# Kernel optimization log

Measured on AMD Instinct MI355X. Metric: run time of the kernel, lower is better.

Reference implementation:

```python
import jax, jax.numpy as jnp
import numpy as np
import math

V, D, L, FF, H, DH, W, DM, T, B = 32000, 1024, 4, 4096, 16, 64, 256, 64, 1024, 1


def rms_norm(x, w):
    return x * jax.lax.rsqrt(jnp.mean(x * x, axis=-1, keepdims=True) + 1e-6) * w


def setup_inputs() -> dict:
    key = jax.random.key(0)
    ks = jax.random.split(key, 16)
    s = 0.02
    return {
        "x": jax.random.randint(ks[0], (B, T), 0, V),
        "embed": jax.random.normal(ks[1], (V, D), jnp.float32) * s,
        "ln_in_w": jnp.ones((D,), jnp.float32),
        "ln1_w": jnp.ones((L, D), jnp.float32),
        "lnd_w": jnp.ones((L, D), jnp.float32),
        "qkv_w": jax.random.normal(ks[2], (L, 3 * H * DH, D), jnp.float32) * s,
        "swa_out_w": jax.random.normal(ks[3], (L, D, H * DH), jnp.float32) * s,
        "k_w": jax.random.normal(ks[4], (L, H * DM, D), jnp.float32) * s,
        "v_w": jax.random.normal(ks[5], (L, H * DM, D), jnp.float32) * s,
        "q_w": jax.random.normal(ks[6], (L, H * DM, D), jnp.float32) * s,
        "beta_w": jax.random.normal(ks[7], (L, H, D), jnp.float32) * s,
        "mem_out_w": jax.random.normal(ks[8], (L, D, H * DM), jnp.float32) * s,
        "gate_w": jax.random.normal(ks[9], (L, D, D), jnp.float32) * s,
        "comb_w": jax.random.normal(ks[10], (L, D, D), jnp.float32) * s,
        "ln2_w": jnp.ones((L, D), jnp.float32),
        "wg": jax.random.normal(ks[11], (L, FF, D), jnp.float32) * s,
        "wu": jax.random.normal(ks[12], (L, FF, D), jnp.float32) * s,
        "wo": jax.random.normal(ks[13], (L, D, FF), jnp.float32) * s,
        "ln_out_w": jnp.ones((D,), jnp.float32),
    }


def _swa(h1, qkv_w, out_w):
    # h1: [B,T,D]
    qkv = jnp.einsum('btd,ed->bte', h1, qkv_w)  # [B,T,3*H*DH]
    q, k, v = jnp.split(qkv, 3, axis=-1)
    q = q.reshape(h1.shape[0], T, H, DH).transpose(0, 2, 1, 3)
    k = k.reshape(h1.shape[0], T, H, DH).transpose(0, 2, 1, 3)
    v = v.reshape(h1.shape[0], T, H, DH).transpose(0, 2, 1, 3)
    scores = jnp.einsum('bhqd,bhkd->bhqk', q, k) * (DH ** -0.5)
    pos = jnp.arange(T)
    dist = pos[:, None] - pos[None, :]
    allowed = (dist >= 0) & (dist < W)  # causal sliding window
    scores = jnp.where(allowed[None, None], scores, -jnp.inf)
    attn = jax.nn.softmax(scores, axis=-1)
    out = jnp.einsum('bhqk,bhkd->bhqd', attn, v)
    out = out.transpose(0, 2, 1, 3).reshape(h1.shape[0], T, H * DH)
    return jnp.einsum('bte,de->btd', out, out_w)


def _delta(h2, k_w, v_w, q_w, beta_w, mem_out_w):
    Bv = h2.shape[0]
    proj = lambda w: jnp.einsum('btd,ed->bte', h2, w).reshape(Bv, T, H, DM).transpose(0, 2, 1, 3)
    keys, values, queries = proj(k_w), proj(v_w), proj(q_w)
    beta = jax.nn.sigmoid(jnp.einsum('btd,hd->bht', h2, beta_w))  # [B,H,T]
    keys = keys / jnp.maximum(jnp.linalg.norm(keys, axis=-1, keepdims=True), 1e-12)
    queries = queries / jnp.maximum(jnp.linalg.norm(queries, axis=-1, keepdims=True), 1e-12)
    log_retain = jnp.log(1.0 - beta + 1e-8)
    cum_log = jnp.cumsum(log_retain, axis=-1)  # [B,H,T]
    log_decay = cum_log[..., :, None] - cum_log[..., None, :]  # [B,H,T,T]
    causal = jnp.triu(jnp.ones((T, T), dtype=bool))  # matches torch.triu mask in source
    decay = jnp.exp(jnp.minimum(log_decay, 0.0)) * causal
    kq = jnp.einsum('bhid,bhjd->bhij', queries, keys) / math.sqrt(DM)
    weights = kq * decay
    out = jnp.einsum('bhij,bhjd->bhid', weights, values)
    out = out + beta[..., None] * values
    out = out.transpose(0, 2, 1, 3).reshape(Bv, T, H * DM)
    return jnp.einsum('bte,de->btd', out, mem_out_w)


def reference(x, embed, ln_in_w, ln1_w, lnd_w, qkv_w, swa_out_w, k_w, v_w, q_w,
              beta_w, mem_out_w, gate_w, comb_w, ln2_w, wg, wu, wo, ln_out_w):
    h = rms_norm(embed[x], ln_in_w)  # [B,T,D]
    for l in range(L):
        h1 = rms_norm(h, ln1_w[l])
        h2 = rms_norm(h, lnd_w[l])
        local = _swa(h1, qkv_w[l], swa_out_w[l])
        global_ctx = _delta(h2, k_w[l], v_w[l], q_w[l], beta_w[l], mem_out_w[l])
        gate = jax.nn.sigmoid(jnp.einsum('btd,ed->bte', h1, gate_w[l]))
        mixed = jnp.einsum('btd,ed->bte', gate * local + (1.0 - gate) * global_ctx, comb_w[l])
        h = h + mixed
        hn = rms_norm(h, ln2_w[l])
        ffn = jnp.einsum('btf,df->btd', jax.nn.silu(jnp.einsum('btd,fd->btf', hn, wg[l])) * jnp.einsum('btd,fd->btf', hn, wu[l]), wo[l])
        h = h + ffn
    logits = jnp.einsum('btd,vd->btv', rms_norm(h, ln_out_w), embed)  # tied head
    return logits
```

## Files before the change

kernel.cpp:

```cpp
#include <hip/hip_runtime.h>

typedef unsigned short u16;
typedef unsigned int   u32;
typedef __attribute__((ext_vector_type(8))) __bf16 bfv8;
typedef __attribute__((ext_vector_type(4))) float  f32x4;

__device__ __forceinline__ u16 f2bf(float f){
  u32 u = __builtin_bit_cast(u32, f);
  return (u16)((u + 0x7FFFu + ((u >> 16) & 1u)) >> 16);
}
__device__ __forceinline__ float bf2f(u16 b){
  return __builtin_bit_cast(float, ((u32)b) << 16);
}
__device__ __forceinline__ u32 pk2(float a, float b){
  return (u32)f2bf(a) | ((u32)f2bf(b) << 16);
}
__device__ __forceinline__ float wsum(float v){
  #pragma unroll
  for (int m = 32; m > 0; m >>= 1) v += __shfl_xor(v, m, 64);
  return v;
}
__device__ __forceinline__ void gload16(const void* g, void* l){
  __builtin_amdgcn_global_load_lds((const __attribute__((address_space(1))) void*)g,
                                   (__attribute__((address_space(3))) void*)l, 16, 0, 0);
}

struct CBatch { const float* s[12]; long long p4[13]; u16* dst; };
__global__ __launch_bounds__(256) void flm_conv(CBatch cb)
{
  long long total = cb.p4[12];
  for (long long i = (long long)blockIdx.x * 256 + threadIdx.x; i < total;
       i += (long long)gridDim.x * 256){
    int t = 0;
    for (int j = 1; j < 12; j++) if (i >= cb.p4[j]) t = j;
    long long il = i - cb.p4[t];
    float4 v = ((const float4*)cb.s[t])[il];
    uint2 p; p.x = pk2(v.x, v.y); p.y = pk2(v.z, v.w);
    ((uint2*)cb.dst)[i] = p;
  }
}

struct GDesc {
  const u16* A; const float* Bw; float* Cf; u16* Cb;
  int lda, ldb, ldc, kbeg, kend, blk0, epi, pad;
};
struct GBatch { GDesc d[6]; int ng, total; };

template<bool BW>
__global__ __launch_bounds__(512) void flm_mgemm(GBatch gb)
{
  constexpr int LDK = BW ? 64 : 72;
  __shared__ u16 sA[128][LDK];
  __shared__ u16 sB[128][LDK];
  const int tid = threadIdx.x, lane = tid & 63, w = tid >> 6;

  const int T = gb.total, bid = blockIdx.x;
  const int q8 = T >> 3, r8 = T & 7, xc = bid & 7, of = bid >> 3;
  const int lin = (xc < r8 ? xc * (q8 + 1) : r8 * (q8 + 1) + (xc - r8) * q8) + of;
  int di = 0;
  #pragma unroll
  for (int i = 1; i < 6; i++) if (i < gb.ng && lin >= gb.d[i].blk0) di = i;
  const GDesc g = gb.d[di];
  const int local = lin - g.blk0;
  const int row0 = (local & 7) * 128;
  const int col0 = (local >> 3) * 128;
  const int wr = (w >> 2) * 64, wc = (w & 3) * 32;

  f32x4 acc[4][2];
  #pragma unroll
  for (int m = 0; m < 4; m++)
    #pragma unroll
    for (int n = 0; n < 2; n++)
      acc[m][n] = (f32x4){0.f, 0.f, 0.f, 0.f};

  const int csw = ((lane & 7) ^ (lane >> 3)) * 8;
  const u16* B16 = (const u16*)g.Bw;

  for (int k0 = g.kbeg; k0 < g.kend; k0 += 64){
    if constexpr (BW){
      const u16* a0 = g.A + (size_t)(row0 + w*16 + (lane>>3)) * g.lda + k0 + csw;
      const u16* b0 = B16 + (size_t)(col0 + w*16 + (lane>>3)) * g.ldb + k0 + csw;
      gload16(a0,                     &sA[w*16    ][0]);
      gload16(a0 + (size_t)8*g.lda,   &sA[w*16 + 8][0]);
      gload16(b0,                     &sB[w*16    ][0]);
      gload16(b0 + (size_t)8*g.ldb,   &sB[w*16 + 8][0]);
    } else {
      #pragma unroll
      for (int i = 0; i < 2; i++){
        int idx = tid + i * 512;
        int r = idx >> 3, c = (idx & 7) * 8;
        *(uint4*)&sA[r][c] = *(const uint4*)(g.A + (size_t)(row0 + r) * g.lda + k0 + c);
      }
      #pragma unroll
      for (int i = 0; i < 4; i++){
        int idx = tid + i * 512;
        int r = idx >> 4, c = (idx & 15) * 4;
        float4 v = *(const float4*)(g.Bw + (size_t)(col0 + r) * g.ldb + k0 + c);
        uint2 p; p.x = pk2(v.x, v.y); p.y = pk2(v.z, v.w);
        *(uint2*)&sB[r][c] = p;
      }
    }
    __syncthreads();
    #pragma unroll
    for (int kk = 0; kk < 2; kk++){
      bfv8 af[4], bfr[2];
      #pragma unroll
      for (int m = 0; m < 4; m++){
        int row = wr + m*16 + (lane & 15);
        if constexpr (BW){
          int slot = (kk*4 + (lane >> 4)) ^ (row & 7);
          af[m] = *(const bfv8*)((const char*)sA + row*128 + slot*16);
        } else {
          af[m] = *(const bfv8*)&sA[row][kk*32 + (lane >> 4) * 8];
        }
      }
      #pragma unroll
      for (int n = 0; n < 2; n++){
        int row = wc + n*16 + (lane & 15);
        if constexpr (BW){
          int slot = (kk*4 + (lane >> 4)) ^ (row & 7);
          bfr[n] = *(const bfv8*)((const char*)sB + row*128 + slot*16);
        } else {
          bfr[n] = *(const bfv8*)&sB[row][kk*32 + (lane >> 4) * 8];
        }
      }
      #pragma unroll
      for (int m = 0; m < 4; m++)
        #pragma unroll
        for (int n = 0; n < 2; n++)
          acc[m][n] = __builtin_amdgcn_mfma_f32_16x16x32_bf16(af[m], bfr[n], acc[m][n], 0, 0, 0);
    }
    __syncthreads();
  }

  #pragma unroll
  for (int m = 0; m < 4; m++){
    int rbase = row0 + wr + m*16 + (lane >> 4) * 4;
    #pragma unroll
    for (int n = 0; n < 2; n++){
      int col = col0 + wc + n*16 + (lane & 15);
      #pragma unroll
      for (int j = 0; j < 4; j++){
        float v = acc[m][n][j];
        size_t o = (size_t)(rbase + j) * g.ldc + col;
        switch (g.epi){
          case 0: g.Cf[o] = v; break;
          case 1: g.Cb[o] = f2bf(v); break;
          default: atomicAdd(&g.Cf[o], v); break;
        }
      }
    }
  }
}

__global__ __launch_bounds__(256) void flm_mix(
    const float* __restrict__ gr, const float* __restrict__ lo,
    const float* __restrict__ gl, u16* __restrict__ o)
{
  int i = blockIdx.x * 256 + threadIdx.x;
  float4 gv = ((const float4*)gr)[i];
  float4 lv = ((const float4*)lo)[i];
  float4 bv = ((const float4*)gl)[i];
  float sx = 1.f/(1.f+expf(-gv.x)), sy = 1.f/(1.f+expf(-gv.y));
  float sz = 1.f/(1.f+expf(-gv.z)), sw = 1.f/(1.f+expf(-gv.w));
  uint2 p;
  p.x = pk2(sx*lv.x + (1.f-sx)*bv.x, sy*lv.y + (1.f-sy)*bv.y);
  p.y = pk2(sz*lv.z + (1.f-sz)*bv.z, sw*lv.w + (1.f-sw)*bv.w);
  ((uint2*)o)[i] = p;
}

__global__ __launch_bounds__(256) void flm_silu(
    const float* __restrict__ gg, const float* __restrict__ uu, u16* __restrict__ o)
{
  int i = blockIdx.x * 256 + threadIdx.x;
  float4 gv = ((const float4*)gg)[i];
  float4 uv = ((const float4*)uu)[i];
  float a = gv.x / (1.f + expf(-gv.x)) * uv.x;
  float b = gv.y / (1.f + expf(-gv.y)) * uv.y;
  float c = gv.z / (1.f + expf(-gv.z)) * uv.z;
  float d = gv.w / (1.f + expf(-gv.w)) * uv.w;
  uint2 p; p.x = pk2(a, b); p.y = pk2(c, d);
  ((uint2*)o)[i] = p;
}

__global__ __launch_bounds__(256) void flm_embed(
    const int* __restrict__ x, const float* __restrict__ embed,
    const float* __restrict__ w, float* __restrict__ h)
{
  int t = blockIdx.x, tid = threadIdx.x;
  int tok = x[t];
  float4 v = ((const float4*)(embed + (size_t)tok * 1024))[tid];
  float ss = v.x*v.x + v.y*v.y + v.z*v.z + v.w*v.w;
  ss = wsum(ss);
  __shared__ float red[4];
  if ((tid & 63) == 0) red[tid >> 6] = ss;
  __syncthreads();
  float inv = rsqrtf((red[0]+red[1]+red[2]+red[3]) * (1.f/1024.f) + 1e-6f);
  float4 wv = ((const float4*)w)[tid];
  float4 o; o.x = v.x*inv*wv.x; o.y = v.y*inv*wv.y; o.z = v.z*inv*wv.z; o.w = v.w*inv*wv.w;
  ((float4*)(h + (size_t)t * 1024))[tid] = o;
}

__global__ __launch_bounds__(256) void flm_rms(
    const float* __restrict__ h, const float* __restrict__ w1, const float* __restrict__ w2,
    u16* __restrict__ o1, u16* __restrict__ o2)
{
  int t = blockIdx.x, tid = threadIdx.x;
  float4 v = ((const float4*)(h + (size_t)t * 1024))[tid];
  float ss = v.x*v.x + v.y*v.y + v.z*v.z + v.w*v.w;
  ss = wsum(ss);
  __shared__ float red[4];
  if ((tid & 63) == 0) red[tid >> 6] = ss;
  __syncthreads();
  float inv = rsqrtf((red[0]+red[1]+red[2]+red[3]) * (1.f/1024.f) + 1e-6f);
  {
    float4 wv = ((const float4*)w1)[tid];
    uint2 p; p.x = pk2(v.x*inv*wv.x, v.y*inv*wv.y); p.y = pk2(v.z*inv*wv.z, v.w*inv*wv.w);
    ((uint2*)(o1 + (size_t)t * 1024))[tid] = p;
  }
  if (o2 != nullptr){
    float4 wv = ((const float4*)w2)[tid];
    uint2 p; p.x = pk2(v.x*inv*wv.x, v.y*inv*wv.y); p.y = pk2(v.z*inv*wv.z, v.w*inv*wv.w);
    ((uint2*)(o2 + (size_t)t * 1024))[tid] = p;
  }
}

__global__ __launch_bounds__(64) void flm_beta(
    const u16* __restrict__ h2, const float* __restrict__ bw, float* __restrict__ beta)
{
  int t = blockIdx.x, lane = threadIdx.x;
  float hv[16];
  #pragma unroll
  for (int i = 0; i < 16; i++) hv[i] = bf2f(h2[(size_t)t*1024 + i*64 + lane]);
  for (int h = 0; h < 16; h++){
    float p = 0.f;
    #pragma unroll
    for (int i = 0; i < 16; i++) p += hv[i] * bw[h*1024 + i*64 + lane];
    p = wsum(p);
    if (lane == 0) beta[t*16 + h] = 1.f / (1.f + expf(-p));
  }
}

__global__ __launch_bounds__(64) void flm_normkq(u16* __restrict__ keys, u16* __restrict__ queries)
{
  int t = blockIdx.x, h = blockIdx.y;
  u16* arr = blockIdx.z ? queries : keys;
  size_t idx = (size_t)t * 1024 + h * 64 + threadIdx.x;
  float v = bf2f(arr[idx]);
  float ss = wsum(v * v);
  float nrm = fmaxf(sqrtf(ss), 1e-12f);
  arr[idx] = f2bf(v / nrm);
}

__global__ __launch_bounds__(256) void flm_attn(
    const u16* __restrict__ qkv,
    const u16* __restrict__ keys, const u16* __restrict__ values, const u16* __restrict__ queries,
    const float* __restrict__ beta, u16* __restrict__ aout, u16* __restrict__ dout)
{
  __shared__ u16 sK[64][72];
  __shared__ u16 sVt[64][72];
  __shared__ u16 sP[4][16][72];
  const int tid = threadIdx.x, lane = tid & 63, w = tid >> 6;
  const int qt = blockIdx.x, h = blockIdx.y;
  const int base = h * 64;
  const int ri = w*16 + (lane>>4)*4;

  if (blockIdx.z == 0){
    bfv8 aq[2];
    {
      int qrow = qt*64 + w*16 + (lane & 15);
      #pragma unroll
      for (int kk = 0; kk < 2; kk++)
        aq[kk] = *(const bfv8*)(qkv + (size_t)qrow*3072 + base + kk*32 + (lane>>4)*8);
    }
    f32x4 acc_o[4];
    float m_r[4], l_r[4];
    #pragma unroll
    for (int n = 0; n < 4; n++) acc_o[n] = (f32x4){0.f,0.f,0.f,0.f};
    #pragma unroll
    for (int r = 0; r < 4; r++){ m_r[r] = -1e30f; l_r[r] = 0.f; }
    const int jt0 = (qt >= 4) ? qt - 4 : 0;

    for (int jt = qt; jt >= jt0; jt--){
      #pragma unroll
      for (int i = 0; i < 2; i++){
        int idx = tid + i*256;
        int r = idx >> 3, c = (idx & 7) * 8;
        uint4 kv = *(const uint4*)(qkv + (size_t)(jt*64+r)*3072 + 1024 + base + c);
        *(uint4*)&sK[r][c] = kv;
        uint4 vv = *(const uint4*)(qkv + (size_t)(jt*64+r)*3072 + 2048 + base + c);
        u16 tmp[8]; *(uint4*)tmp = vv;
        #pragma unroll
        for (int e = 0; e < 8; e++) sVt[c+e][r] = tmp[e];
      }
      __syncthreads();

      f32x4 sv[4];
      #pragma unroll
      for (int n = 0; n < 4; n++) sv[n] = (f32x4){0.f,0.f,0.f,0.f};
      #pragma unroll
      for (int kk = 0; kk < 2; kk++){
        #pragma unroll
        for (int n = 0; n < 4; n++){
          bfv8 bk = *(const bfv8*)&sK[n*16 + (lane & 15)][(lane>>4)*8 + kk*32];
          sv[n] = __builtin_amdgcn_mfma_f32_16x16x32_bf16(aq[kk], bk, sv[n], 0, 0, 0);
        }
      }
      #pragma unroll
      for (int n = 0; n < 4; n++){
        int cj = n*16 + (lane & 15);
        #pragma unroll
        for (int r = 0; r < 4; r++){
          float s = sv[n][r] * 0.125f;
          if (jt == qt)      { if (cj > ri + r) s = -1e30f; }
          else if (jt == jt0 && qt - jt0 == 4) { if (cj <= ri + r) s = -1e30f; }
          sv[n][r] = s;
        }
      }
      float pv[4][4], scl[4];
      #pragma unroll
      for (int r = 0; r < 4; r++){
        float mx = -1e30f;
        #pragma unroll
        for (int n = 0; n < 4; n++) mx = fmaxf(mx, sv[n][r]);
        #pragma unroll
        for (int m = 1; m < 16; m <<= 1) mx = fmaxf(mx, __shfl_xor(mx, m, 64));
        float mn = fmaxf(m_r[r], mx);
        float sc = expf(m_r[r] - mn);
        m_r[r] = mn; scl[r] = sc;
        float rs = 0.f;
        #pragma unroll
        for (int n = 0; n < 4; n++){ float p = expf(sv[n][r] - mn); pv[n][r] = p; rs += p; }
        #pragma unroll
        for (int m = 1; m < 16; m <<= 1) rs += __shfl_xor(rs, m, 64);
        l_r[r] = l_r[r] * sc + rs;
      }
      #pragma unroll
      for (int n = 0; n < 4; n++){
        #pragma unroll
        for (int r = 0; r < 4; r++){
          acc_o[n][r] *= scl[r];
          sP[w][(lane>>4)*4 + r][n*16 + (lane & 15)] = f2bf(pv[n][r]);
        }
      }
      #pragma unroll
      for (int kk = 0; kk < 2; kk++){
        bfv8 ap = *(const bfv8*)&sP[w][lane & 15][(lane>>4)*8 + kk*32];
        #pragma unroll
        for (int n = 0; n < 4; n++){
          bfv8 bv = *(const bfv8*)&sVt[n*16 + (lane & 15)][(lane>>4)*8 + kk*32];
          acc_o[n] = __builtin_amdgcn_mfma_f32_16x16x32_bf16(ap, bv, acc_o[n], 0, 0, 0);
        }
      }
      __syncthreads();
    }

    #pragma unroll
    for (int n = 0; n < 4; n++){
      int col = base + n*16 + (lane & 15);
      #pragma unroll
      for (int r = 0; r < 4; r++){
        int row = qt*64 + ri + r;
        aout[(size_t)row*1024 + col] = f2bf(acc_o[n][r] / l_r[r]);
      }
    }
  } else {
    bfv8 aq[2];
    {
      int qrow = qt*64 + w*16 + (lane & 15);
      #pragma unroll
      for (int kk = 0; kk < 2; kk++)
        aq[kk] = *(const bfv8*)(queries + (size_t)qrow*1024 + base + kk*32 + (lane>>4)*8);
    }
    f32x4 acc_o[4];
    #pragma unroll
    for (int n = 0; n < 4; n++) acc_o[n] = (f32x4){0.f,0.f,0.f,0.f};

    for (int jt = qt; jt < 16; jt++){
      #pragma unroll
      for (int i = 0; i < 2; i++){
        int idx = tid + i*256;
        int r = idx >> 3, c = (idx & 7) * 8;
        uint4 kv = *(const uint4*)(keys + (size_t)(jt*64+r)*1024 + base + c);
        *(uint4*)&sK[r][c] = kv;
        uint4 vv = *(const uint4*)(values + (size_t)(jt*64+r)*1024 + base + c);
        u16 tmp[8]; *(uint4*)tmp = vv;
        #pragma unroll
        for (int e = 0; e < 8; e++) sVt[c+e][r] = tmp[e];
      }
      __syncthreads();

      f32x4 sv[4];
      #pragma unroll
      for (int n = 0; n < 4; n++) sv[n] = (f32x4){0.f,0.f,0.f,0.f};
      #pragma unroll
      for (int kk = 0; kk < 2; kk++){
        #pragma unroll
        for (int n = 0; n < 4; n++){
          bfv8 bk = *(const bfv8*)&sK[n*16 + (lane & 15)][(lane>>4)*8 + kk*32];
          sv[n] = __builtin_amdgcn_mfma_f32_16x16x32_bf16(aq[kk], bk, sv[n], 0, 0, 0);
        }
      }
      #pragma unroll
      for (int n = 0; n < 4; n++){
        int cj = n*16 + (lane & 15);
        #pragma unroll
        for (int r = 0; r < 4; r++){
          float p = sv[n][r] * 0.125f;
          if (jt == qt && cj < ri + r) p = 0.f;
          sP[w][(lane>>4)*4 + r][n*16 + (lane & 15)] = f2bf(p);
        }
      }
      #pragma unroll
      for (int kk = 0; kk < 2; kk++){
        bfv8 ap = *(const bfv8*)&sP[w][lane & 15][(lane>>4)*8 + kk*32];
        #pragma unroll
        for (int n = 0; n < 4; n++){
          bfv8 bv = *(const bfv8*)&sVt[n*16 + (lane & 15)][(lane>>4)*8 + kk*32];
          acc_o[n] = __builtin_amdgcn_mfma_f32_16x16x32_bf16(ap, bv, acc_o[n], 0, 0, 0);
        }
      }
      __syncthreads();
    }

    #pragma unroll
    for (int n = 0; n < 4; n++){
      int col = base + n*16 + (lane & 15);
      #pragma unroll
      for (int r = 0; r < 4; r++){
        int row = qt*64 + ri + r;
        float b = beta[row*16 + h];
        float v = bf2f(values[(size_t)row*1024 + col]);
        dout[(size_t)row*1024 + col] = f2bf(acc_o[n][r] + b * v);
      }
    }
  }
}

static GDesc mkd(const u16* A, int lda, const float* Bw, int ldb,
                 float* Cf, u16* Cb, int ldc,
                 int kbeg, int kend, int blk0, int epi){
  GDesc d; d.A=A; d.Bw=Bw; d.Cf=Cf; d.Cb=Cb;
  d.lda=lda; d.ldb=ldb; d.ldc=ldc; d.kbeg=kbeg; d.kend=kend; d.blk0=blk0; d.epi=epi; d.pad=0;
  return d;
}

extern "C" void kernel_launch(void* const* d_in, const int* in_sizes, int n_in,
                              void* d_out, int out_size, void* d_ws, size_t ws_size,
                              hipStream_t stream)
{
  (void)in_sizes; (void)n_in; (void)out_size;
  const int*   x        = (const int*)d_in[0];
  const float* embed    = (const float*)d_in[1];
  const float* ln_in_w  = (const float*)d_in[2];
  const float* ln1_w    = (const float*)d_in[3];
  const float* lnd_w    = (const float*)d_in[4];
  const float* qkv_w    = (const float*)d_in[5];
  const float* swa_out_w= (const float*)d_in[6];
  const float* k_w      = (const float*)d_in[7];
  const float* v_w      = (const float*)d_in[8];
  const float* q_w      = (const float*)d_in[9];
  const float* beta_w   = (const float*)d_in[10];
  const float* mem_out_w= (const float*)d_in[11];
  const float* gate_w   = (const float*)d_in[12];
  const float* comb_w   = (const float*)d_in[13];
  const float* ln2_w    = (const float*)d_in[14];
  const float* wg       = (const float*)d_in[15];
  const float* wu       = (const float*)d_in[16];
  const float* wo       = (const float*)d_in[17];
  const float* ln_out_w = (const float*)d_in[18];
  float* out = (float*)d_out;

  char* ws = (char*)d_ws;
  const size_t KB = 1024, MB = 1u << 20;
  float* h       = (float*)(ws + 0);
  u16*   h1      = (u16*)  (ws + 4*MB);
  u16*   h2      = (u16*)  (ws + 6*MB);
  u16*   qkvb    = (u16*)  (ws + 8*MB);
  u16*   keys    = (u16*)  (ws + 14*MB);
  u16*   values  = (u16*)  (ws + 16*MB);
  u16*   queries = (u16*)  (ws + 18*MB);
  float* beta    = (float*)(ws + 20*MB);
  u16*   attn    = (u16*)  (ws + 20*MB + 256*KB);
  u16*   delt    = (u16*)  (ws + 22*MB + 256*KB);
  float* localb  = (float*)(ws + 24*MB + 256*KB);
  float* globb   = (float*)(ws + 28*MB + 256*KB);
  u16*   mcomb   = (u16*)  (ws + 32*MB + 256*KB);
  u16*   hn      = (u16*)  (ws + 36*MB);
  float* gbuf    = (float*)(ws + 40*MB);
  float* g       = (float*)(ws + 4*MB);
  float* u       = (float*)(ws + 20*MB);
  u16*   sbuf    = (u16*)  (ws + 36*MB);

  u16* wb = (u16*)(ws + 44*MB);
  size_t off = 0; auto nx = [&](size_t n){ size_t o = off; off += n; return o; };
  const size_t nEmb = 32768000ULL, nQkv = 12582912ULL, nSq = 4194304ULL, nFf = 16777216ULL;
  u16* wemb  = wb + nx(nEmb);
  u16* wqkv  = wb + nx(nQkv);
  u16* wswa  = wb + nx(nSq);
  u16* wk    = wb + nx(nSq);
  u16* wv    = wb + nx(nSq);
  u16* wq    = wb + nx(nSq);
  u16* wmem  = wb + nx(nSq);
  u16* wgate = wb + nx(nSq);
  u16* wcomb = wb + nx(nSq);
  u16* wwg   = wb + nx(nFf);
  u16* wwu   = wb + nx(nFf);
  u16* wwo   = wb + nx(nFf);
  const size_t NEED = 44*MB + off * 2;
  const bool bw = (ws_size >= NEED);

  auto MG = [&](int nblk, GBatch& gbv){
    if (bw) flm_mgemm<true><<<nblk, 512, 0, stream>>>(gbv);
    else    flm_mgemm<false><<<nblk, 512, 0, stream>>>(gbv);
  };

  if (bw){
    CBatch cb;
    const float* srcs[12] = {embed, qkv_w, swa_out_w, k_w, v_w, q_w,
                             mem_out_w, gate_w, comb_w, wg, wu, wo};
    const size_t ns[12] = {nEmb, nQkv, nSq, nSq, nSq, nSq, nSq, nSq, nSq, nFf, nFf, nFf};
    long long acc4 = 0;
    for (int i = 0; i < 12; i++){ cb.s[i] = srcs[i]; cb.p4[i] = acc4; acc4 += (long long)(ns[i] >> 2); }
    cb.p4[12] = acc4; cb.dst = wb;
    flm_conv<<<2048, 256, 0, stream>>>(cb);
  }

  flm_embed<<<1024, 256, 0, stream>>>(x, embed, ln_in_w, h);

  for (int l = 0; l < 4; l++){
    const size_t lq = (size_t)l * 3145728, ls = (size_t)l * 1048576, lf = (size_t)l * 4194304;
    const float* Wqkv  = bw ? (const float*)(wqkv  + lq) : qkv_w     + lq;
    const float* Wk    = bw ? (const float*)(wk    + ls) : k_w       + ls;
    const float* Wv    = bw ? (const float*)(wv    + ls) : v_w       + ls;
    const float* Wq    = bw ? (const float*)(wq    + ls) : q_w       + ls;
    const float* Wswa  = bw ? (const float*)(wswa  + ls) : swa_out_w + ls;
    const float* Wmem  = bw ? (const float*)(wmem  + ls) : mem_out_w + ls;
    const float* Wgate = bw ? (const float*)(wgate + ls) : gate_w    + ls;
    const float* Wcomb = bw ? (const float*)(wcomb + ls) : comb_w    + ls;
    const float* Wwg   = bw ? (const float*)(wwg   + lf) : wg        + lf;
    const float* Wwu   = bw ? (const float*)(wwu   + lf) : wu        + lf;
    const float* Wwo   = bw ? (const float*)(wwo   + lf) : wo        + lf;

    flm_rms<<<1024, 256, 0, stream>>>(h, ln1_w + l*1024, lnd_w + l*1024, h1, h2);

    {
      GBatch gb;
      gb.d[0] = mkd(h1, 1024, Wqkv, 1024, nullptr, qkvb, 3072, 0, 1024, 0, 1);
      gb.d[1] = mkd(h2, 1024, Wk, 1024, nullptr, keys, 1024, 0, 1024, 192, 1);
      gb.d[2] = mkd(h2, 1024, Wv, 1024, nullptr, values, 1024, 0, 1024, 256, 1);
      gb.d[3] = mkd(h2, 1024, Wq, 1024, nullptr, queries, 1024, 0, 1024, 320, 1);
      gb.d[4] = mkd(h1, 1024, Wgate, 1024, gbuf, nullptr, 1024, 0, 1024, 384, 0);
      gb.d[5] = gb.d[4]; gb.d[5].blk0 = 0x7fffffff;
      gb.ng = 5; gb.total = 448;
      MG(448, gb);
    }
    flm_beta<<<1024, 64, 0, stream>>>(h2, beta_w + (size_t)l*16*1024, beta);
    flm_normkq<<<dim3(1024, 16, 2), 64, 0, stream>>>(keys, queries);
    flm_attn<<<dim3(16, 16, 2), 256, 0, stream>>>(qkvb, keys, values, queries, beta, attn, delt);

    {
      GBatch gb;
      gb.d[0] = mkd(attn, 1024, Wswa, 1024, localb, nullptr, 1024, 0, 1024, 0, 0);
      gb.d[1] = mkd(delt, 1024, Wmem, 1024, globb, nullptr, 1024, 0, 1024, 64, 0);
      gb.d[2] = gb.d[1]; gb.d[2].blk0 = 0x7fffffff;
      gb.d[3] = gb.d[2]; gb.d[4] = gb.d[2]; gb.d[5] = gb.d[2];
      gb.ng = 2; gb.total = 128;
      MG(128, gb);
    }
    flm_mix<<<1024, 256, 0, stream>>>(gbuf, localb, globb, mcomb);
    {
      GBatch gb;
      gb.d[0] = mkd(mcomb, 1024, Wcomb, 1024, h, nullptr, 1024, 0, 512, 0, 5);
      gb.d[1] = mkd(mcomb, 1024, Wcomb, 1024, h, nullptr, 1024, 512, 1024, 64, 5);
      gb.d[2] = gb.d[1]; gb.d[2].blk0 = 0x7fffffff;
      gb.d[3] = gb.d[2]; gb.d[4] = gb.d[2]; gb.d[5] = gb.d[2];
      gb.ng = 2; gb.total = 128;
      MG(128, gb);
    }
    flm_rms<<<1024, 256, 0, stream>>>(h, ln2_w + l*1024, nullptr, hn, nullptr);
    {
      GBatch gb;
      gb.d[0] = mkd(hn, 1024, Wwg, 1024, g, nullptr, 4096, 0, 1024, 0, 0);
      gb.d[1] = mkd(hn, 1024, Wwu, 1024, u, nullptr, 4096, 0, 1024, 256, 0);
      gb.d[2] = gb.d[1]; gb.d[2].blk0 = 0x7fffffff;
      gb.d[3] = gb.d[2]; gb.d[4] = gb.d[2]; gb.d[5] = gb.d[2];
      gb.ng = 2; gb.total = 512;
      MG(512, gb);
    }
    flm_silu<<<4096, 256, 0, stream>>>(g, u, sbuf);
    {
      GBatch gb;
      for (int s = 0; s < 4; s++)
        gb.d[s] = mkd(sbuf, 4096, Wwo, 4096, h, nullptr, 1024, s*1024, (s+1)*1024, s*64, 5);
      gb.d[4] = gb.d[3]; gb.d[4].blk0 = 0x7fffffff;
      gb.d[5] = gb.d[4];
      gb.ng = 4; gb.total = 256;
      MG(256, gb);
    }
  }

  flm_rms<<<1024, 256, 0, stream>>>(h, ln_out_w, nullptr, hn, nullptr);
  {
    GBatch gb;
    gb.d[0] = mkd(hn, 1024, bw ? (const float*)wemb : embed, 1024, out, nullptr, 32000,
                  0, 1024, 0, 0);
    gb.d[1] = gb.d[0]; gb.d[1].blk0 = 0x7fffffff;
    gb.d[2] = gb.d[1]; gb.d[3] = gb.d[1]; gb.d[4] = gb.d[1]; gb.d[5] = gb.d[1];
    gb.ng = 1; gb.total = 2000;
    MG(2000, gb);
  }
}
```

Measured before the change: 1.018 ms.

## Widen GEMM warp tiles, split-K small GEMMs, fuse beta with kq norm, segment conv

The batched GEMM drops from 512 to 256 threads per block, so each wave computes a 64x64 sub-tile with 16 accumulators instead of 64x32, which raises register reuse of A and B fragments. The swa-out/mem-out and comb GEMMs are split along K into more blocks that accumulate atomically into zeroed buffers, giving more parallelism on the 128-block launches. The beta and key/query normalization kernels are fused into one launch, and the weight conversion kernel indexes each segment by blockIdx.y instead of searching segment offsets per element. The trade-offs are fewer waves per block for latency hiding, higher register pressure, an extra memset, and nondeterministic atomic accumulation.

Result: slower. 1.141 ms (+12.0%).

```diff
diff --git a/kernel.cpp b/kernel.cpp
--- a/kernel.cpp
+++ b/kernel.cpp
@@ -28,15 +28,16 @@
 struct CBatch { const float* s[12]; long long p4[13]; u16* dst; };
 __global__ __launch_bounds__(256) void flm_conv(CBatch cb)
 {
-  long long total = cb.p4[12];
-  for (long long i = (long long)blockIdx.x * 256 + threadIdx.x; i < total;
+  const int seg = blockIdx.y;
+  const long long base = cb.p4[seg];
+  const long long n4 = cb.p4[seg + 1] - base;
+  const float* __restrict__ src = cb.s[seg];
+  uint2* __restrict__ dst = (uint2*)cb.dst + base;
+  for (long long i = (long long)blockIdx.x * 256 + threadIdx.x; i < n4;
        i += (long long)gridDim.x * 256){
-    int t = 0;
-    for (int j = 1; j < 12; j++) if (i >= cb.p4[j]) t = j;
-    long long il = i - cb.p4[t];
-    float4 v = ((const float4*)cb.s[t])[il];
+    float4 v = ((const float4*)src)[i];
     uint2 p; p.x = pk2(v.x, v.y); p.y = pk2(v.z, v.w);
-    ((uint2*)cb.dst)[i] = p;
+    dst[i] = p;
   }
 }
 
@@ -47,7 +48,7 @@
 struct GBatch { GDesc d[6]; int ng, total; };
 
 template<bool BW>
-__global__ __launch_bounds__(512) void flm_mgemm(GBatch gb)
+__global__ __launch_bounds__(256) void flm_mgemm(GBatch gb)
 {
   constexpr int LDK = BW ? 64 : 72;
   __shared__ u16 sA[128][LDK];
@@ -64,36 +65,37 @@
   const int local = lin - g.blk0;
   const int row0 = (local & 7) * 128;
   const int col0 = (local >> 3) * 128;
-  const int wr = (w >> 2) * 64, wc = (w & 3) * 32;
-
-  f32x4 acc[4][2];
+  const int wr = (w >> 1) * 64, wc = (w & 1) * 64;
+
+  f32x4 acc[4][4];
   #pragma unroll
   for (int m = 0; m < 4; m++)
     #pragma unroll
-    for (int n = 0; n < 2; n++)
+    for (int n = 0; n < 4; n++)
       acc[m][n] = (f32x4){0.f, 0.f, 0.f, 0.f};
 
-  const int csw = ((lane & 7) ^ (lane >> 3)) * 8;
+  const int sub = lane >> 3;
+  const int csw = ((lane & 7) ^ sub) * 8;
   const u16* B16 = (const u16*)g.Bw;
 
   for (int k0 = g.kbeg; k0 < g.kend; k0 += 64){
     if constexpr (BW){
-      const u16* a0 = g.A + (size_t)(row0 + w*16 + (lane>>3)) * g.lda + k0 + csw;
-      const u16* b0 = B16 + (size_t)(col0 + w*16 + (lane>>3)) * g.ldb + k0 + csw;
-      gload16(a0,                     &sA[w*16    ][0]);
-      gload16(a0 + (size_t)8*g.lda,   &sA[w*16 + 8][0]);
-      gload16(b0,                     &sB[w*16    ][0]);
-      gload16(b0 + (size_t)8*g.ldb,   &sB[w*16 + 8][0]);
+      #pragma unroll
+      for (int i = 0; i < 4; i++){
+        int rr = w*32 + i*8;
+        gload16(g.A + (size_t)(row0 + rr + sub) * g.lda + k0 + csw, &sA[rr][0]);
+        gload16(B16 + (size_t)(col0 + rr + sub) * g.ldb + k0 + csw, &sB[rr][0]);
+      }
     } else {
       #pragma unroll
-      for (int i = 0; i < 2; i++){
-        int idx = tid + i * 512;
+      for (int i = 0; i < 4; i++){
+        int idx = tid + i * 256;
         int r = idx >> 3, c = (idx & 7) * 8;
         *(uint4*)&sA[r][c] = *(const uint4*)(g.A + (size_t)(row0 + r) * g.lda + k0 + c);
       }
       #pragma unroll
-      for (int i = 0; i < 4; i++){
-        int idx = tid + i * 512;
+      for (int i = 0; i < 8; i++){
+        int idx = tid + i * 256;
         int r = idx >> 4, c = (idx & 15) * 4;
         float4 v = *(const float4*)(g.Bw + (size_t)(col0 + r) * g.ldb + k0 + c);
         uint2 p; p.x = pk2(v.x, v.y); p.y = pk2(v.z, v.w);
@@ -103,7 +105,7 @@
     __syncthreads();
     #pragma unroll
     for (int kk = 0; kk < 2; kk++){
-      bfv8 af[4], bfr[2];
+      bfv8 af[4], bfr[4];
       #pragma unroll
       for (int m = 0; m < 4; m++){
         int row = wr + m*16 + (lane & 15);
@@ -115,7 +117,7 @@
         }
       }
       #pragma unroll
-      for (int n = 0; n < 2; n++){
+      for (int n = 0; n < 4; n++){
         int row = wc + n*16 + (lane & 15);
         if constexpr (BW){
           int slot = (kk*4 + (lane >> 4)) ^ (row & 7);
@@ -127,7 +129,7 @@
       #pragma unroll
       for (int m = 0; m < 4; m++)
         #pragma unroll
-        for (int n = 0; n < 2; n++)
+        for (int n = 0; n < 4; n++)
           acc[m][n] = __builtin_amdgcn_mfma_f32_16x16x32_bf16(af[m], bfr[n], acc[m][n], 0, 0, 0);
     }
     __syncthreads();
@@ -137,7 +139,7 @@
   for (int m = 0; m < 4; m++){
     int rbase = row0 + wr + m*16 + (lane >> 4) * 4;
     #pragma unroll
-    for (int n = 0; n < 2; n++){
+    for (int n = 0; n < 4; n++){
       int col = col0 + wc + n*16 + (lane & 15);
       #pragma unroll
       for (int j = 0; j < 4; j++){
@@ -225,8 +227,9 @@
   }
 }
 
-__global__ __launch_bounds__(64) void flm_beta(
-    const u16* __restrict__ h2, const float* __restrict__ bw, float* __restrict__ beta)
+__global__ __launch_bounds__(64) void flm_betanorm(
+    const u16* __restrict__ h2, const float* __restrict__ bw, float* __restrict__ beta,
+    u16* __restrict__ keys, u16* __restrict__ queries)
 {
   int t = blockIdx.x, lane = threadIdx.x;
   float hv[16];
@@ -239,17 +242,16 @@
     p = wsum(p);
     if (lane == 0) beta[t*16 + h] = 1.f / (1.f + expf(-p));
   }
-}
-
-__global__ __launch_bounds__(64) void flm_normkq(u16* __restrict__ keys, u16* __restrict__ queries)
-{
-  int t = blockIdx.x, h = blockIdx.y;
-  u16* arr = blockIdx.z ? queries : keys;
-  size_t idx = (size_t)t * 1024 + h * 64 + threadIdx.x;
-  float v = bf2f(arr[idx]);
-  float ss = wsum(v * v);
-  float nrm = fmaxf(sqrtf(ss), 1e-12f);
-  arr[idx] = f2bf(v / nrm);
+  #pragma unroll
+  for (int h = 0; h < 16; h++){
+    size_t idx = (size_t)t * 1024 + h * 64 + lane;
+    float v = bf2f(keys[idx]);
+    float nrm = fmaxf(sqrtf(wsum(v * v)), 1e-12f);
+    keys[idx] = f2bf(v / nrm);
+    float q = bf2f(queries[idx]);
+    float qn = fmaxf(sqrtf(wsum(q * q)), 1e-12f);
+    queries[idx] = f2bf(q / qn);
+  }
 }
 
 __global__ __launch_bounds__(256) void flm_attn(
@@ -511,8 +513,8 @@
   const bool bw = (ws_size >= NEED);
 
   auto MG = [&](int nblk, GBatch& gbv){
-    if (bw) flm_mgemm<true><<<nblk, 512, 0, stream>>>(gbv);
-    else    flm_mgemm<false><<<nblk, 512, 0, stream>>>(gbv);
+    if (bw) flm_mgemm<true><<<nblk, 256, 0, stream>>>(gbv);
+    else    flm_mgemm<false><<<nblk, 256, 0, stream>>>(gbv);
   };
 
   if (bw){
@@ -523,7 +525,7 @@
     long long acc4 = 0;
     for (int i = 0; i < 12; i++){ cb.s[i] = srcs[i]; cb.p4[i] = acc4; acc4 += (long long)(ns[i] >> 2); }
     cb.p4[12] = acc4; cb.dst = wb;
-    flm_conv<<<2048, 256, 0, stream>>>(cb);
+    flm_conv<<<dim3(512, 12), 256, 0, stream>>>(cb);
   }
 
   flm_embed<<<1024, 256, 0, stream>>>(x, embed, ln_in_w, h);
@@ -555,28 +557,30 @@
       gb.ng = 5; gb.total = 448;
       MG(448, gb);
     }
-    flm_beta<<<1024, 64, 0, stream>>>(h2, beta_w + (size_t)l*16*1024, beta);
-    flm_normkq<<<dim3(1024, 16, 2), 64, 0, stream>>>(keys, queries);
+    flm_betanorm<<<1024, 64, 0, stream>>>(h2, beta_w + (size_t)l*16*1024, beta, keys, queries);
     flm_attn<<<dim3(16, 16, 2), 256, 0, stream>>>(qkvb, keys, values, queries, beta, attn, delt);
 
+    hipMemsetAsync(localb, 0, 8*MB, stream);
     {
       GBatch gb;
-      gb.d[0] = mkd(attn, 1024, Wswa, 1024, localb, nullptr, 1024, 0, 1024, 0, 0);
-      gb.d[1] = mkd(delt, 1024, Wmem, 1024, globb, nullptr, 1024, 0, 1024, 64, 0);
-      gb.d[2] = gb.d[1]; gb.d[2].blk0 = 0x7fffffff;
-      gb.d[3] = gb.d[2]; gb.d[4] = gb.d[2]; gb.d[5] = gb.d[2];
-      gb.ng = 2; gb.total = 128;
-      MG(128, gb);
+      gb.d[0] = mkd(attn, 1024, Wswa, 1024, localb, nullptr, 1024, 0,   512,  0,   5);
+      gb.d[1] = mkd(attn, 1024, Wswa, 1024, localb, nullptr, 1024, 512, 1024, 64,  5);
+      gb.d[2] = mkd(delt, 1024, Wmem, 1024, globb,  nullptr, 1024, 0,   512,  128, 5);
+      gb.d[3] = mkd(delt, 1024, Wmem, 1024, globb,  nullptr, 1024, 512, 1024, 192, 5);
+      gb.d[4] = gb.d[3]; gb.d[4].blk0 = 0x7fffffff;
+      gb.d[5] = gb.d[4];
+      gb.ng = 4; gb.total = 256;
+      MG(256, gb);
     }
     flm_mix<<<1024, 256, 0, stream>>>(gbuf, localb, globb, mcomb);
     {
       GBatch gb;
-      gb.d[0] = mkd(mcomb, 1024, Wcomb, 1024, h, nullptr, 1024, 0, 512, 0, 5);
-      gb.d[1] = mkd(mcomb, 1024, Wcomb, 1024, h, nullptr, 1024, 512, 1024, 64, 5);
-      gb.d[2] = gb.d[1]; gb.d[2].blk0 = 0x7fffffff;
-      gb.d[3] = gb.d[2]; gb.d[4] = gb.d[2]; gb.d[5] = gb.d[2];
-      gb.ng = 2; gb.total = 128;
-      MG(128, gb);
+      for (int s = 0; s < 4; s++)
+        gb.d[s] = mkd(mcomb, 1024, Wcomb, 1024, h, nullptr, 1024, s*256, (s+1)*256, s*64, 5);
+      gb.d[4] = gb.d[3]; gb.d[4].blk0 = 0x7fffffff;
+      gb.d[5] = gb.d[4];
+      gb.ng = 4; gb.total = 256;
+      MG(256, gb);
     }
     flm_rms<<<1024, 256, 0, stream>>>(h, ln2_w + l*1024, nullptr, hn, nullptr);
     {
```

## Store FFN gate/up in bf16, fuse beta and kq-norm, segment weight conversion

Applied to the files above, without the earlier changes.

The FFN gate and up GEMMs now write bf16 outputs instead of fp32, and the SiLU kernel reads bf16. This halves the intermediate traffic, at the cost of rounding the pre-activation to bf16. The beta and key/query normalization kernels are merged into one launch. The weight-conversion kernel now uses a 2D grid with one segment per y index, which removes the per-element segment search.

Measured after the change: 1.007 ms. No clear change (-1.0%).

```diff
diff --git a/kernel.cpp b/kernel.cpp
--- a/kernel.cpp
+++ b/kernel.cpp
@@ -28,15 +28,16 @@
 struct CBatch { const float* s[12]; long long p4[13]; u16* dst; };
 __global__ __launch_bounds__(256) void flm_conv(CBatch cb)
 {
-  long long total = cb.p4[12];
-  for (long long i = (long long)blockIdx.x * 256 + threadIdx.x; i < total;
+  const int seg = blockIdx.y;
+  const long long base = cb.p4[seg];
+  const long long n4 = cb.p4[seg + 1] - base;
+  const float* __restrict__ src = cb.s[seg];
+  uint2* __restrict__ dst = (uint2*)cb.dst + base;
+  for (long long i = (long long)blockIdx.x * 256 + threadIdx.x; i < n4;
        i += (long long)gridDim.x * 256){
-    int t = 0;
-    for (int j = 1; j < 12; j++) if (i >= cb.p4[j]) t = j;
-    long long il = i - cb.p4[t];
-    float4 v = ((const float4*)cb.s[t])[il];
+    float4 v = ((const float4*)src)[i];
     uint2 p; p.x = pk2(v.x, v.y); p.y = pk2(v.z, v.w);
-    ((uint2*)cb.dst)[i] = p;
+    dst[i] = p;
   }
 }
 
@@ -170,15 +171,19 @@
 }
 
 __global__ __launch_bounds__(256) void flm_silu(
-    const float* __restrict__ gg, const float* __restrict__ uu, u16* __restrict__ o)
+    const u16* __restrict__ gg, const u16* __restrict__ uu, u16* __restrict__ o)
 {
   int i = blockIdx.x * 256 + threadIdx.x;
-  float4 gv = ((const float4*)gg)[i];
-  float4 uv = ((const float4*)uu)[i];
-  float a = gv.x / (1.f + expf(-gv.x)) * uv.x;
-  float b = gv.y / (1.f + expf(-gv.y)) * uv.y;
-  float c = gv.z / (1.f + expf(-gv.z)) * uv.z;
-  float d = gv.w / (1.f + expf(-gv.w)) * uv.w;
+  uint2 gv = ((const uint2*)gg)[i];
+  uint2 uv = ((const uint2*)uu)[i];
+  float g0 = bf2f((u16)gv.x), g1 = bf2f((u16)(gv.x >> 16));
+  float g2 = bf2f((u16)gv.y), g3 = bf2f((u16)(gv.y >> 16));
+  float u0 = bf2f((u16)uv.x), u1 = bf2f((u16)(uv.x >> 16));
+  float u2 = bf2f((u16)uv.y), u3 = bf2f((u16)(uv.y >> 16));
+  float a = g0 / (1.f + expf(-g0)) * u0;
+  float b = g1 / (1.f + expf(-g1)) * u1;
+  float c = g2 / (1.f + expf(-g2)) * u2;
+  float d = g3 / (1.f + expf(-g3)) * u3;
   uint2 p; p.x = pk2(a, b); p.y = pk2(c, d);
   ((uint2*)o)[i] = p;
 }
@@ -225,8 +230,9 @@
   }
 }
 
-__global__ __launch_bounds__(64) void flm_beta(
-    const u16* __restrict__ h2, const float* __restrict__ bw, float* __restrict__ beta)
+__global__ __launch_bounds__(64) void flm_betanorm(
+    const u16* __restrict__ h2, const float* __restrict__ bw, float* __restrict__ beta,
+    u16* __restrict__ keys, u16* __restrict__ queries)
 {
   int t = blockIdx.x, lane = threadIdx.x;
   float hv[16];
@@ -239,17 +245,16 @@
     p = wsum(p);
     if (lane == 0) beta[t*16 + h] = 1.f / (1.f + expf(-p));
   }
-}
-
-__global__ __launch_bounds__(64) void flm_normkq(u16* __restrict__ keys, u16* __restrict__ queries)
-{
-  int t = blockIdx.x, h = blockIdx.y;
-  u16* arr = blockIdx.z ? queries : keys;
-  size_t idx = (size_t)t * 1024 + h * 64 + threadIdx.x;
-  float v = bf2f(arr[idx]);
-  float ss = wsum(v * v);
-  float nrm = fmaxf(sqrtf(ss), 1e-12f);
-  arr[idx] = f2bf(v / nrm);
+  #pragma unroll
+  for (int h = 0; h < 16; h++){
+    size_t idx = (size_t)t * 1024 + h * 64 + lane;
+    float v = bf2f(keys[idx]);
+    float nrm = fmaxf(sqrtf(wsum(v * v)), 1e-12f);
+    keys[idx] = f2bf(v / nrm);
+    float q = bf2f(queries[idx]);
+    float qn = fmaxf(sqrtf(wsum(q * q)), 1e-12f);
+    queries[idx] = f2bf(q / qn);
+  }
 }
 
 __global__ __launch_bounds__(256) void flm_attn(
@@ -488,8 +493,8 @@
   u16*   mcomb   = (u16*)  (ws + 32*MB + 256*KB);
   u16*   hn      = (u16*)  (ws + 36*MB);
   float* gbuf    = (float*)(ws + 40*MB);
-  float* g       = (float*)(ws + 4*MB);
-  float* u       = (float*)(ws + 20*MB);
+  u16*   g16     = (u16*)  (ws + 4*MB);
+  u16*   u16b    = (u16*)  (ws + 12*MB);
   u16*   sbuf    = (u16*)  (ws + 36*MB);
 
   u16* wb = (u16*)(ws + 44*MB);
@@ -523,7 +528,7 @@
     long long acc4 = 0;
     for (int i = 0; i < 12; i++){ cb.s[i] = srcs[i]; cb.p4[i] = acc4; acc4 += (long long)(ns[i] >> 2); }
     cb.p4[12] = acc4; cb.dst = wb;
-    flm_conv<<<2048, 256, 0, stream>>>(cb);
+    flm_conv<<<dim3(1024, 12), 256, 0, stream>>>(cb);
   }
 
   flm_embed<<<1024, 256, 0, stream>>>(x, embed, ln_in_w, h);
@@ -555,8 +560,7 @@
       gb.ng = 5; gb.total = 448;
       MG(448, gb);
     }
-    flm_beta<<<1024, 64, 0, stream>>>(h2, beta_w + (size_t)l*16*1024, beta);
-    flm_normkq<<<dim3(1024, 16, 2), 64, 0, stream>>>(keys, queries);
+    flm_betanorm<<<1024, 64, 0, stream>>>(h2, beta_w + (size_t)l*16*1024, beta, keys, queries);
     flm_attn<<<dim3(16, 16, 2), 256, 0, stream>>>(qkvb, keys, values, queries, beta, attn, delt);
 
     {
@@ -581,14 +585,14 @@
     flm_rms<<<1024, 256, 0, stream>>>(h, ln2_w + l*1024, nullptr, hn, nullptr);
     {
       GBatch gb;
-      gb.d[0] = mkd(hn, 1024, Wwg, 1024, g, nullptr, 4096, 0, 1024, 0, 0);
-      gb.d[1] = mkd(hn, 1024, Wwu, 1024, u, nullptr, 4096, 0, 1024, 256, 0);
+      gb.d[0] = mkd(hn, 1024, Wwg, 1024, nullptr, g16, 4096, 0, 1024, 0, 1);
+      gb.d[1] = mkd(hn, 1024, Wwu, 1024, nullptr, u16b, 4096, 0, 1024, 256, 1);
       gb.d[2] = gb.d[1]; gb.d[2].blk0 = 0x7fffffff;
       gb.d[3] = gb.d[2]; gb.d[4] = gb.d[2]; gb.d[5] = gb.d[2];
       gb.ng = 2; gb.total = 512;
       MG(512, gb);
     }
-    flm_silu<<<4096, 256, 0, stream>>>(g, u, sbuf);
+    flm_silu<<<4096, 256, 0, stream>>>(g16, u16b, sbuf);
     {
       GBatch gb;
       for (int s = 0; s < 4; s++)
```
